# Performance work log

Measured on AMD Instinct MI355X. Metric: run time of the kernel, lower is better.

Reference implementation:

```python
import jax, jax.numpy as jnp
import numpy as np

NUM_EMBEDDINGS = 1024
EMBEDDING_DIM = 64
COMMITMENT_COST = 0.25
DECAY = 0.99
EPSILON = 1e-05
N_TOKENS = 131072


def setup_inputs() -> dict:
    key = jax.random.key(0)
    k1, k2, k3 = jax.random.split(key, 3)
    inputs = jax.random.normal(k1, (N_TOKENS, EMBEDDING_DIM), dtype=jnp.float32)
    embed_w = jax.random.normal(k2, (NUM_EMBEDDINGS, EMBEDDING_DIM), dtype=jnp.float32)
    ema_w = jax.random.normal(k3, (NUM_EMBEDDINGS, EMBEDDING_DIM), dtype=jnp.float32)
    ema_cluster_size = jnp.zeros((NUM_EMBEDDINGS,), dtype=jnp.float32)
    return {"inputs": inputs, "embed_w": embed_w, "ema_w": ema_w,
            "ema_cluster_size": ema_cluster_size}


def reference(inputs, embed_w, ema_w, ema_cluster_size):
    K = embed_w.shape[0]
    # squared L2 distances [N, K]
    distances = (jnp.sum(inputs ** 2, axis=1, keepdims=True)
                 + jnp.sum(embed_w ** 2, axis=1)
                 - 2.0 * inputs @ embed_w.T)
    encoding_indices = jnp.argmin(distances, axis=1)          # [N]
    encodings = jax.nn.one_hot(encoding_indices, K, dtype=inputs.dtype)  # [N, K]

    # EMA updates (training branch in the torch module)
    cluster_size = ema_cluster_size * DECAY + (1.0 - DECAY) * jnp.sum(encodings, axis=0)
    n = jnp.sum(cluster_size)
    cluster_size = (cluster_size + EPSILON) / (n + K * EPSILON) * n  # Laplace smoothing
    dw = jax.ops.segment_sum(inputs, encoding_indices, num_segments=K)  # == encodings.T @ inputs
    ema_w_new = ema_w * DECAY + (1.0 - DECAY) * dw
    embedding_new = ema_w_new / cluster_size[:, None]

    quantized = embedding_new[encoding_indices]               # == encodings @ embedding_new
    e_latent_loss = jnp.mean(0.5 * jnp.sum((jax.lax.stop_gradient(quantized) - inputs) ** 2, axis=1))
    loss = COMMITMENT_COST * e_latent_loss
    quantized = inputs + jax.lax.stop_gradient(quantized - inputs)  # straight-through

    avg_probs = jnp.mean(encodings, axis=0)
    perplexity = jnp.exp(-jnp.sum(avg_probs * jnp.log(avg_probs + 1e-10)))
    return (loss, quantized, perplexity, encodings)
```

## Files before the change

kernel.cpp:

```cpp
#include <hip/hip_runtime.h>
#include <hip/hip_fp16.h>

#define N_TOK 131072
#define KCODES 1024
#define DIM 64
#define QUANT_OFF 1
#define PERP_OFF 8388609
#define ENC_OFF ((size_t)8388610)
#define EPS_SUSPECT 4e-3f

typedef __attribute__((ext_vector_type(8))) unsigned short ushort8v;
typedef __attribute__((ext_vector_type(8))) _Float16 half8v;
typedef __attribute__((ext_vector_type(4))) float f32x4;

__device__ __forceinline__ float wave_reduce_sum(float v) {
    #pragma unroll
    for (int o = 32; o > 0; o >>= 1) v += __shfl_xor(v, o, 64);
    return v;
}

__device__ __forceinline__ void cvt8h(const float4 a, const float4 b,
                                      half8v* h, half8v* l) {
    float f[8] = {a.x, a.y, a.z, a.w, b.x, b.y, b.z, b.w};
    #pragma unroll
    for (int j = 0; j < 8; ++j) {
        _Float16 hh = (_Float16)f[j];
        float fh = (float)hh;
        _Float16 ll = (_Float16)(f[j] - fh);
        (*h)[j] = hh;
        (*l)[j] = ll;
    }
}

__global__ void k0_prep(const float* __restrict__ ew, float* __restrict__ cbuf,
                        unsigned short* __restrict__ ewh, unsigned short* __restrict__ ewl,
                        float* __restrict__ dwacc, unsigned* __restrict__ suspcnt) {
    int tid = threadIdx.x;
    int lane = tid & 63;
    int wg = blockIdx.x * 4 + (tid >> 6);
    int gt = blockIdx.x * 256 + tid;
    if (gt == 0) *suspcnt = 0u;
    #pragma unroll
    for (int z = 0; z < 8; ++z) {
        int e = gt * 8 + z;
        float v = ew[e];
        _Float16 hh = (_Float16)v;
        float fh = (float)hh;
        _Float16 ll = (_Float16)(v - fh);
        unsigned short uh, ul;
        __builtin_memcpy(&uh, &hh, 2);
        __builtin_memcpy(&ul, &ll, 2);
        ewh[e] = uh;
        ewl[e] = ul;
        dwacc[e] = 0.0f;
    }
    #pragma unroll
    for (int k = 0; k < 8; ++k) {
        int row = wg * 8 + k;
        float v = ew[row * 64 + lane];
        float s = wave_reduce_sum(v * v);
        if (lane == 0) cbuf[row] = 0.5f * s;
    }
}

__global__ __launch_bounds__(256) void k1_argmin(
        const float* __restrict__ x, const unsigned short* __restrict__ ewh,
        const unsigned short* __restrict__ ewl, const float* __restrict__ cbuf,
        float* __restrict__ out, unsigned* __restrict__ idxbuf,
        unsigned* __restrict__ susp, unsigned* __restrict__ suspcnt) {
    __shared__ unsigned short EH[128 * 64];
    __shared__ unsigned short EL[128 * 64];
    __shared__ float scc[128];

    int tid = threadIdx.x;
    int lane = tid & 63;
    int wv = tid >> 6;
    int l15 = lane & 15;
    int l4 = lane >> 4;
    size_t t0 = (size_t)blockIdx.x * 128;
    size_t t0w = t0 + (size_t)wv * 32;

    half8v ah[2][2], al[2][2];
    #pragma unroll
    for (int rt = 0; rt < 2; ++rt) {
        const float* xp = x + (t0w + rt * 16 + l15) * 64 + l4 * 8;
        #pragma unroll
        for (int s = 0; s < 2; ++s) {
            float4 a = *(const float4*)(xp + s * 32);
            float4 b = *(const float4*)(xp + s * 32 + 4);
            cvt8h(a, b, &ah[rt][s], &al[rt][s]);
        }
    }

    float m1[2][4], m2[2][4];
    int i1[2][4], i2[2][4];
    #pragma unroll
    for (int rt = 0; rt < 2; ++rt)
        #pragma unroll
        for (int r = 0; r < 4; ++r) {
            m1[rt][r] = -3.4e38f; m2[rt][r] = -3.4e38f;
            i1[rt][r] = 0; i2[rt][r] = 0;
        }

    for (int ch = 0; ch < 8; ++ch) {
        int c0 = ch * 128;
        {
            int r = tid >> 1, h = tid & 1;
            const unsigned short* gh = ewh + (size_t)(c0 + r) * 64 + h * 32;
            const unsigned short* gl = ewl + (size_t)(c0 + r) * 64 + h * 32;
            #pragma unroll
            for (int q = 0; q < 4; ++q) {
                ushort8v hv = *(const ushort8v*)(gh + q * 8);
                ushort8v lv = *(const ushort8v*)(gl + q * 8);
                int byteoff = (r * 128 + h * 64 + q * 16) ^ ((r & 7) << 4);
                *(ushort8v*)((char*)EH + byteoff) = hv;
                *(ushort8v*)((char*)EL + byteoff) = lv;
            }
            if (tid < 128) scc[tid] = cbuf[c0 + tid];
        }
        __syncthreads();

        {
            float2 z; z.x = 0.0f; z.y = 0.0f;
            float* base = out + ENC_OFF + (t0 + (size_t)ch * 16) * 1024;
            #pragma unroll 4
            for (int u = 0; u < 32; ++u) {
                int idx = u * 256 + tid;
                int row = idx >> 9;
                int c2 = idx & 511;
                *(float2*)(base + (size_t)row * 1024 + c2 * 2) = z;
            }
        }

        #pragma unroll 2
        for (int ct = 0; ct < 8; ++ct) {
            int crow = ct * 16 + l15;
            int swz = (crow & 7) << 4;
            int b0 = (crow * 128 + l4 * 16) ^ swz;
            int b1 = (crow * 128 + 64 + l4 * 16) ^ swz;
            half8v bh0 = *(half8v*)((char*)EH + b0);
            half8v bl0 = *(half8v*)((char*)EL + b0);
            half8v bh1 = *(half8v*)((char*)EH + b1);
            half8v bl1 = *(half8v*)((char*)EL + b1);
            float sccv = scc[crow];
            int cid = c0 + crow;
            #pragma unroll
            for (int rt = 0; rt < 2; ++rt) {
                f32x4 acc = {0.f, 0.f, 0.f, 0.f};
                acc = __builtin_amdgcn_mfma_f32_16x16x32_f16(ah[rt][0], bh0, acc, 0, 0, 0);
                acc = __builtin_amdgcn_mfma_f32_16x16x32_f16(al[rt][0], bh0, acc, 0, 0, 0);
                acc = __builtin_amdgcn_mfma_f32_16x16x32_f16(ah[rt][0], bl0, acc, 0, 0, 0);
                acc = __builtin_amdgcn_mfma_f32_16x16x32_f16(al[rt][0], bl0, acc, 0, 0, 0);
                acc = __builtin_amdgcn_mfma_f32_16x16x32_f16(ah[rt][1], bh1, acc, 0, 0, 0);
                acc = __builtin_amdgcn_mfma_f32_16x16x32_f16(al[rt][1], bh1, acc, 0, 0, 0);
                acc = __builtin_amdgcn_mfma_f32_16x16x32_f16(ah[rt][1], bl1, acc, 0, 0, 0);
                acc = __builtin_amdgcn_mfma_f32_16x16x32_f16(al[rt][1], bl1, acc, 0, 0, 0);
                #pragma unroll
                for (int r = 0; r < 4; ++r) {
                    float sc = acc[r] - sccv;
                    if (sc > m1[rt][r]) {
                        m2[rt][r] = m1[rt][r]; i2[rt][r] = i1[rt][r];
                        m1[rt][r] = sc; i1[rt][r] = cid;
                    } else if (sc > m2[rt][r]) {
                        m2[rt][r] = sc; i2[rt][r] = cid;
                    }
                }
            }
        }
        __syncthreads();
    }

    #pragma unroll
    for (int rt = 0; rt < 2; ++rt)
        #pragma unroll
        for (int r = 0; r < 4; ++r) {
            float m1v = m1[rt][r], m2v = m2[rt][r];
            int i1v = i1[rt][r], i2v = i2[rt][r];
            #pragma unroll
            for (int o = 1; o < 16; o <<= 1) {
                float b1 = __shfl_xor(m1v, o, 64); int bi1 = __shfl_xor(i1v, o, 64);
                float b2 = __shfl_xor(m2v, o, 64); int bi2 = __shfl_xor(i2v, o, 64);
                if (b1 > m1v || (b1 == m1v && bi1 < i1v)) {
                    float c2v; int c2i;
                    if (m1v > b2 || (m1v == b2 && i1v < bi2)) { c2v = m1v; c2i = i1v; }
                    else { c2v = b2; c2i = bi2; }
                    m1v = b1; i1v = bi1; m2v = c2v; i2v = c2i;
                } else {
                    if (b1 > m2v || (b1 == m2v && bi1 < i2v)) { m2v = b1; i2v = bi1; }
                }
            }
            if (l15 == 0) {
                size_t tok = t0w + rt * 16 + l4 * 4 + r;
                idxbuf[tok] = (unsigned)i1v;
                if (m2v >= m1v - EPS_SUSPECT) {
                    unsigned p = atomicAdd(suspcnt, 1u);
                    susp[p] = (unsigned)tok;
                }
            }
        }
}

__global__ void k1s_resolve(const float* __restrict__ x, const float* __restrict__ ew,
                            const float* __restrict__ cbuf, const unsigned* __restrict__ susp,
                            const unsigned* __restrict__ suspcnt, unsigned* __restrict__ idxbuf) {
    int lane = threadIdx.x & 63;
    int wid = blockIdx.x * 4 + (threadIdx.x >> 6);
    unsigned n = *suspcnt;
    for (unsigned s = wid; s < n; s += 256) {
        unsigned tok = susp[s];
        float4 xr[16];
        const float4* xp = (const float4*)(x + (size_t)tok * 64);
        #pragma unroll
        for (int q = 0; q < 16; ++q) xr[q] = xp[q];
        float best = -3.4e38f;
        int bidx = 0;
        for (int rr = 0; rr < 16; ++rr) {
            int code = rr * 64 + lane;
            const float4* ep = (const float4*)(ew + (size_t)code * 64);
            float d = 0.0f;
            #pragma unroll
            for (int q = 0; q < 16; ++q) {
                float4 xv = xr[q];
                float4 e = ep[q];
                d = fmaf(xv.x, e.x, d); d = fmaf(xv.y, e.y, d);
                d = fmaf(xv.z, e.z, d); d = fmaf(xv.w, e.w, d);
            }
            float sc = d - cbuf[code];
            if (sc > best) { best = sc; bidx = code; }
        }
        #pragma unroll
        for (int o = 1; o < 64; o <<= 1) {
            float vo = __shfl_xor(best, o, 64);
            int io = __shfl_xor(bidx, o, 64);
            if (vo > best || (vo == best && io < bidx)) { best = vo; bidx = io; }
        }
        if (lane == 0) idxbuf[tok] = (unsigned)bidx;
    }
}

__global__ void k1h_hist(unsigned* __restrict__ idxbuf, unsigned* __restrict__ blockhist) {
    __shared__ unsigned hist[1024];
    int tid = threadIdx.x;
    #pragma unroll
    for (int q = 0; q < 4; ++q) hist[q * 256 + tid] = 0u;
    __syncthreads();
    if (tid < 128) {
        size_t tok = (size_t)blockIdx.x * 128 + tid;
        unsigned bin = idxbuf[tok];
        unsigned rank = atomicAdd(&hist[bin], 1u);
        idxbuf[tok] = bin | (rank << 10);
    }
    __syncthreads();
    #pragma unroll
    for (int q = 0; q < 4; ++q)
        blockhist[(size_t)blockIdx.x * 1024 + q * 256 + tid] = hist[q * 256 + tid];
}

__global__ void k2a_scan(const unsigned* __restrict__ blockhist,
                         unsigned* __restrict__ blockbase,
                         unsigned* __restrict__ counts) {
    int lane = threadIdx.x & 63;
    int bin = blockIdx.x * 4 + (threadIdx.x >> 6);
    unsigned v[16];
    unsigned s = 0;
    #pragma unroll
    for (int j = 0; j < 16; ++j) v[j] = blockhist[(size_t)(lane * 16 + j) * 1024 + bin];
    #pragma unroll
    for (int j = 0; j < 16; ++j) { unsigned t = v[j]; v[j] = s; s += t; }
    unsigned inc = s;
    for (int o = 1; o < 64; o <<= 1) {
        unsigned n = __shfl_up(inc, o, 64);
        if (lane >= o) inc += n;
    }
    unsigned excl = inc - s;
    #pragma unroll
    for (int j = 0; j < 16; ++j)
        blockbase[(size_t)(lane * 16 + j) * 1024 + bin] = excl + v[j];
    if (lane == 63) counts[bin] = inc;
}

__global__ void k2_stats(const float* __restrict__ ema_cs, const unsigned* __restrict__ counts,
                         float* __restrict__ smoothed, unsigned* __restrict__ offsets,
                         float* __restrict__ out) {
    __shared__ unsigned sc[1024];
    __shared__ float sf[1024];
    int t = threadIdx.x;
    unsigned cnt = counts[t];
    float cs = 0.99f * ema_cs[t] + 0.01f * (float)cnt;

    sf[t] = cs; __syncthreads();
    for (int o = 512; o > 0; o >>= 1) { if (t < o) sf[t] += sf[t + o]; __syncthreads(); }
    float n = sf[0];
    __syncthreads();
    smoothed[t] = (cs + 1e-5f) / (n + 1024.0f * 1e-5f) * n;

    sc[t] = cnt; __syncthreads();
    for (int o = 1; o < 1024; o <<= 1) {
        unsigned v = (t >= o) ? sc[t - o] : 0u;
        __syncthreads();
        sc[t] += v;
        __syncthreads();
    }
    offsets[t] = sc[t] - cnt;

    float p = (float)cnt / 131072.0f;
    sf[t] = p * logf(p + 1e-10f); __syncthreads();
    for (int o = 512; o > 0; o >>= 1) { if (t < o) sf[t] += sf[t + o]; __syncthreads(); }
    if (t == 0) out[PERP_OFF] = expf(-sf[0]);
}

__global__ void k3_scatter(const unsigned* __restrict__ idxbuf,
                           const unsigned* __restrict__ offsets,
                           const unsigned* __restrict__ blockbase,
                           int* __restrict__ toklist, int* __restrict__ clustid,
                           float* __restrict__ out) {
    int i = blockIdx.x * 256 + threadIdx.x;
    unsigned v = idxbuf[i];
    unsigned bin = v & 1023u;
    unsigned rank = v >> 10;
    unsigned pos = offsets[bin] + blockbase[(size_t)(i >> 7) * 1024 + bin] + rank;
    toklist[pos] = i;
    clustid[pos] = (int)bin;
    out[ENC_OFF + (size_t)i * 1024 + bin] = 1.0f;
}

__global__ void k4a_dw(const float* __restrict__ x, const int* __restrict__ toklist,
                       const int* __restrict__ clustid, float* __restrict__ dwacc) {
    int lane = threadIdx.x & 63, w = threadIdx.x >> 6;
    int p0 = blockIdx.x * 128 + w * 32;
    int cur = clustid[p0];
    float acc = 0.0f;
    #pragma unroll 4
    for (int t = 0; t < 32; ++t) {
        int pos = p0 + t;
        int c = clustid[pos];
        int tok = toklist[pos];
        float v = x[(size_t)tok * 64 + lane];
        if (c != cur) {
            atomicAdd(&dwacc[(size_t)cur * 64 + lane], acc);
            acc = 0.0f; cur = c;
        }
        acc += v;
    }
    atomicAdd(&dwacc[(size_t)cur * 64 + lane], acc);
}

__global__ void k4b_emb(const float* __restrict__ emaw, const float* __restrict__ dwacc,
                        const float* __restrict__ smoothed, float* __restrict__ embnew) {
    int t = blockIdx.x * 256 + threadIdx.x;
    int k = t >> 6;
    embnew[t] = (emaw[t] * 0.99f + 0.01f * dwacc[t]) / smoothed[k];
}

__global__ void k5_output(const float* __restrict__ x, const float* __restrict__ embnew,
                          const unsigned* __restrict__ idxbuf, float* __restrict__ out,
                          float* __restrict__ partials) {
    __shared__ float red[4];
    int tid = threadIdx.x;
    int gid = blockIdx.x * 256 + tid;
    size_t i = (size_t)(gid >> 4);
    int c = (gid & 15) * 4;
    unsigned ii = idxbuf[i] & 1023u;
    float4 xv = *(const float4*)(x + i * 64 + c);
    float4 q = *(const float4*)(embnew + (size_t)ii * 64 + c);
    float* o = out + QUANT_OFF + i * 64 + c;
    float d0 = q.x - xv.x, d1 = q.y - xv.y, d2 = q.z - xv.z, d3 = q.w - xv.w;
    o[0] = xv.x + d0; o[1] = xv.y + d1; o[2] = xv.z + d2; o[3] = xv.w + d3;
    float ls = d0 * d0 + d1 * d1 + d2 * d2 + d3 * d3;
    ls = wave_reduce_sum(ls);
    if ((tid & 63) == 0) red[tid >> 6] = ls;
    __syncthreads();
    if (tid == 0) partials[blockIdx.x] = red[0] + red[1] + red[2] + red[3];
}

__global__ void k6_loss(const float* __restrict__ partials, float* __restrict__ out) {
    __shared__ float red[4];
    int tid = threadIdx.x;
    float s = 0.0f;
    #pragma unroll 8
    for (int j = 0; j < 32; ++j) s += partials[tid + j * 256];
    s = wave_reduce_sum(s);
    if ((tid & 63) == 0) red[tid >> 6] = s;
    __syncthreads();
    if (tid == 0) out[0] = 0.125f * (red[0] + red[1] + red[2] + red[3]) / 131072.0f;
}

extern "C" void kernel_launch(void* const* d_in, const int* in_sizes, int n_in,
                              void* d_out, int out_size, void* d_ws, size_t ws_size,
                              hipStream_t stream) {
    const float* x     = (const float*)d_in[0];
    const float* ew    = (const float*)d_in[1];
    const float* emaw  = (const float*)d_in[2];
    const float* emacs = (const float*)d_in[3];
    float* out = (float*)d_out;
    float* wsf = (float*)d_ws;

    float*          cbuf      = wsf;
    float*          smoothed  = wsf + 1024;
    unsigned*       offsets   = (unsigned*)(wsf + 2048);
    unsigned*       counts    = (unsigned*)(wsf + 3072);
    float*          partials  = wsf + 4096;
    unsigned*       suspcnt   = (unsigned*)(wsf + 12288);
    unsigned*       idxbuf    = (unsigned*)(wsf + 12352);
    unsigned*       susp      = idxbuf + N_TOK;
    int*            toklist   = (int*)(susp + N_TOK);
    int*            clustid   = toklist + N_TOK;
    float*          dwacc     = wsf + 12352 + 4 * N_TOK;
    float*          embnew    = dwacc + 65536;
    unsigned*       blockhist = (unsigned*)(embnew + 65536);
    unsigned*       blockbase = blockhist + 1024 * 1024;
    unsigned short* ewh       = (unsigned short*)(blockbase + 1024 * 1024);
    unsigned short* ewl       = ewh + 65536;

    hipLaunchKernelGGL(k0_prep,    dim3(32),   dim3(256),  0, stream, ew, cbuf, ewh, ewl, dwacc, suspcnt);
    hipLaunchKernelGGL(k1_argmin,  dim3(1024), dim3(256),  0, stream, x, ewh, ewl, cbuf, out, idxbuf, susp, suspcnt);
    hipLaunchKernelGGL(k1s_resolve,dim3(64),   dim3(256),  0, stream, x, ew, cbuf, susp, suspcnt, idxbuf);
    hipLaunchKernelGGL(k1h_hist,   dim3(1024), dim3(256),  0, stream, idxbuf, blockhist);
    hipLaunchKernelGGL(k2a_scan,   dim3(256),  dim3(256),  0, stream, blockhist, blockbase, counts);
    hipLaunchKernelGGL(k2_stats,   dim3(1),    dim3(1024), 0, stream, emacs, counts, smoothed, offsets, out);
    hipLaunchKernelGGL(k3_scatter, dim3(512),  dim3(256),  0, stream, idxbuf, offsets, blockbase, toklist, clustid, out);
    hipLaunchKernelGGL(k4a_dw,     dim3(1024), dim3(256),  0, stream, x, toklist, clustid, dwacc);
    hipLaunchKernelGGL(k4b_emb,    dim3(256),  dim3(256),  0, stream, emaw, dwacc, smoothed, embnew);
    hipLaunchKernelGGL(k5_output,  dim3(8192), dim3(256),  0, stream, x, embnew, idxbuf, out, partials);
    hipLaunchKernelGGL(k6_loss,    dim3(1),    dim3(256),  0, stream, partials, out);
}
```

Baseline: 734.2 us.

## Drop low*low MFMA terms, widen encoding zero stores, use wave-level reductions in stats

In the distance kernel, the two low-times-low fp16 MFMA products of the split-precision dot product are removed, cutting MFMA work by a quarter. This slightly lowers the accuracy of the distance scores, which could change argmin choices on near ties. The zero-fill of the one-hot encodings switches from float2 to float4 stores, with the unaligned ends of each 16-row tile handled separately. The stats kernel replaces its shared-memory tree reductions and Hillis-Steele scan with wave shuffle reductions and scans, cutting the number of block barriers.

```diff
diff --git a/kernel.cpp b/kernel.cpp
--- a/kernel.cpp
+++ b/kernel.cpp
@@ -121,15 +121,17 @@
         __syncthreads();
 
         {
-            float2 z; z.x = 0.0f; z.y = 0.0f;
             float* base = out + ENC_OFF + (t0 + (size_t)ch * 16) * 1024;
+            float4 z4; z4.x = z4.y = z4.z = z4.w = 0.0f;
+            float2 z2; z2.x = z2.y = 0.0f;
+            float4* b4 = (float4*)(base + 2);
             #pragma unroll 4
-            for (int u = 0; u < 32; ++u) {
-                int idx = u * 256 + tid;
-                int row = idx >> 9;
-                int c2 = idx & 511;
-                *(float2*)(base + (size_t)row * 1024 + c2 * 2) = z;
-            }
+            for (int u = 0; u < 16; ++u) {
+                int slot = u * 256 + tid;
+                if (slot < 4095) b4[slot] = z4;
+            }
+            if (tid == 0) *(float2*)base = z2;
+            if (tid == 255) *(float2*)(base + 16382) = z2;
         }
 
         #pragma unroll 2
@@ -150,11 +152,9 @@
                 acc = __builtin_amdgcn_mfma_f32_16x16x32_f16(ah[rt][0], bh0, acc, 0, 0, 0);
                 acc = __builtin_amdgcn_mfma_f32_16x16x32_f16(al[rt][0], bh0, acc, 0, 0, 0);
                 acc = __builtin_amdgcn_mfma_f32_16x16x32_f16(ah[rt][0], bl0, acc, 0, 0, 0);
-                acc = __builtin_amdgcn_mfma_f32_16x16x32_f16(al[rt][0], bl0, acc, 0, 0, 0);
                 acc = __builtin_amdgcn_mfma_f32_16x16x32_f16(ah[rt][1], bh1, acc, 0, 0, 0);
                 acc = __builtin_amdgcn_mfma_f32_16x16x32_f16(al[rt][1], bh1, acc, 0, 0, 0);
                 acc = __builtin_amdgcn_mfma_f32_16x16x32_f16(ah[rt][1], bl1, acc, 0, 0, 0);
-                acc = __builtin_amdgcn_mfma_f32_16x16x32_f16(al[rt][1], bl1, acc, 0, 0, 0);
                 #pragma unroll
                 for (int r = 0; r < 4; ++r) {
                     float sc = acc[r] - sccv;
@@ -282,31 +282,51 @@
 __global__ void k2_stats(const float* __restrict__ ema_cs, const unsigned* __restrict__ counts,
                          float* __restrict__ smoothed, unsigned* __restrict__ offsets,
                          float* __restrict__ out) {
-    __shared__ unsigned sc[1024];
-    __shared__ float sf[1024];
+    __shared__ float sfw[16];
+    __shared__ unsigned scw[16];
+    __shared__ float nsh;
     int t = threadIdx.x;
+    int lane = t & 63, w = t >> 6;
     unsigned cnt = counts[t];
     float cs = 0.99f * ema_cs[t] + 0.01f * (float)cnt;
 
-    sf[t] = cs; __syncthreads();
-    for (int o = 512; o > 0; o >>= 1) { if (t < o) sf[t] += sf[t + o]; __syncthreads(); }
-    float n = sf[0];
-    __syncthreads();
+    float s = wave_reduce_sum(cs);
+    if (lane == 0) sfw[w] = s;
+    __syncthreads();
+    if (t == 0) {
+        float n = 0.f;
+        #pragma unroll
+        for (int j = 0; j < 16; ++j) n += sfw[j];
+        nsh = n;
+    }
+    __syncthreads();
+    float n = nsh;
     smoothed[t] = (cs + 1e-5f) / (n + 1024.0f * 1e-5f) * n;
 
-    sc[t] = cnt; __syncthreads();
-    for (int o = 1; o < 1024; o <<= 1) {
-        unsigned v = (t >= o) ? sc[t - o] : 0u;
-        __syncthreads();
-        sc[t] += v;
-        __syncthreads();
-    }
-    offsets[t] = sc[t] - cnt;
+    unsigned inc = cnt;
+    #pragma unroll
+    for (int o = 1; o < 64; o <<= 1) {
+        unsigned v = __shfl_up(inc, o, 64);
+        if (lane >= o) inc += v;
+    }
+    if (lane == 63) scw[w] = inc;
+    __syncthreads();
+    unsigned wb = 0;
+    #pragma unroll
+    for (int j = 0; j < 16; ++j) if (j < w) wb += scw[j];
+    offsets[t] = wb + inc - cnt;
 
     float p = (float)cnt / 131072.0f;
-    sf[t] = p * logf(p + 1e-10f); __syncthreads();
-    for (int o = 512; o > 0; o >>= 1) { if (t < o) sf[t] += sf[t + o]; __syncthreads(); }
-    if (t == 0) out[PERP_OFF] = expf(-sf[0]);
+    float term = p * logf(p + 1e-10f);
+    float ps = wave_reduce_sum(term);
+    if (lane == 0) sfw[w] = ps;
+    __syncthreads();
+    if (t == 0) {
+        float e = 0.f;
+        #pragma unroll
+        for (int j = 0; j < 16; ++j) e += sfw[j];
+        out[PERP_OFF] = expf(-e);
+    }
 }
 
 __global__ void k3_scatter(const unsigned* __restrict__ idxbuf,
```

After: 731.5 us. Within noise of the previous version (-0.4%).
